# Kernel optimization log

Hardware: AMD Instinct MI355X
Metric: run time of the kernel (lower is better)

The kernel has to match this reference:

```python
import jax, jax.numpy as jnp
import numpy as np

N_NODES = 50000
N_RELS = 20          # raw relations; enriched total = 2*N_RELS + 1
N_EDGES = 500000
EMB = 16
N_CLASSES = 16
N_BASES = 40


def setup_inputs() -> dict:
    key = jax.random.key(0)
    ks = jax.random.split(key, 8)
    R_tot = 2 * N_RELS + 1
    src = jax.random.randint(ks[0], (N_EDGES,), 0, N_NODES)
    dst = jax.random.randint(ks[1], (N_EDGES,), 0, N_NODES)
    rel = jax.random.randint(ks[2], (N_EDGES,), 0, N_RELS)
    scale = 0.05
    comps1 = jax.random.normal(ks[3], (R_tot, N_BASES), jnp.float32) * scale
    bases1 = jax.random.normal(ks[4], (N_BASES, N_NODES, EMB), jnp.float32) * scale
    comps2 = jax.random.normal(ks[5], (R_tot, N_BASES), jnp.float32) * scale
    bases2 = jax.random.normal(ks[6], (N_BASES, EMB, N_CLASSES), jnp.float32) * scale
    bias1 = jnp.zeros((EMB,), jnp.float32)
    bias2 = jnp.zeros((N_CLASSES,), jnp.float32)
    return {"src": src, "dst": dst, "rel": rel,
            "comps1": comps1, "bases1": bases1,
            "comps2": comps2, "bases2": bases2,
            "bias1": bias1, "bias2": bias2}


def reference(src, dst, rel, comps1, bases1, comps2, bases2, bias1, bias2):
    N = bases1.shape[1]
    emb = bases1.shape[2]
    R_tot = comps1.shape[0]
    R = (R_tot - 1) // 2

    # enrich: originals + inverses + self-loops (relation 2R)
    loop = jnp.arange(N)
    s = jnp.concatenate([src, dst, loop])           # [E_tot]
    o = jnp.concatenate([dst, src, loop])
    r = jnp.concatenate([rel, rel + R, jnp.full((N,), 2 * R, rel.dtype)])

    # row-normalization of the vertical graph: value = 1 / count(row = r*N + s)
    seg = r * N + s
    cnt = jax.ops.segment_sum(jnp.ones_like(s, jnp.float32), seg,
                              num_segments=R_tot * N)
    v = 1.0 / cnt[seg]                               # [E_tot]

    # layer 1: basis-decomposed weights [R_tot, N, emb]
    w1 = jnp.einsum('rb,bne->rne', comps1, bases1)
    # hor_graph @ w1.view(R*N, emb): h[s] += v * w1[r, o]
    h = jnp.zeros((N, emb), w1.dtype).at[s].add(v[:, None] * w1[r, o])
    h = jax.nn.relu(h + bias1)

    # ver_graph @ h: hv[r, s] += v * h[o]  -> [R_tot, N, emb]
    hv = jnp.zeros((R_tot, N, emb), h.dtype).at[r, s].add(v[:, None] * h[o])

    # layer 2: basis-decomposed weights [R_tot, emb, C]; bmm + sum over relations
    w2 = jnp.einsum('rb,bec->rec', comps2, bases2)
    out = jnp.einsum('rne,rec->nc', hv, w2) + bias2  # [N, C]
    return out
```

## Files before the change

kernel.cpp:

```cpp
#include <hip/hip_runtime.h>

#define N_NODES 50000
#define N_RELSR 20
#define R_TOT   41
#define N_EDGES 500000
#define EMB     16
#define NCLS    16
#define NB      40
#define E_TOT   (2 * N_EDGES + N_NODES)
#define NE_COL  (N_NODES * EMB)
#define NBLK_N  ((N_NODES + 255) / 256)

__device__ __forceinline__ void edge_decode(int i, const int* __restrict__ src,
                                            const int* __restrict__ dst,
                                            const int* __restrict__ rel,
                                            int& s, int& o, int& r) {
    if (i < N_EDGES) {
        s = src[i]; o = dst[i]; r = rel[i];
    } else if (i < 2 * N_EDGES) {
        int j = i - N_EDGES;
        s = dst[j]; o = src[j]; r = rel[j] + N_RELSR;
    } else {
        int n = i - 2 * N_EDGES;
        s = n; o = n; r = 2 * N_RELSR;
    }
}


__global__ void k_count(const int* __restrict__ src, const int* __restrict__ dst,
                        const int* __restrict__ rel, int2* __restrict__ cnt2,
                        int* __restrict__ rank) {
    int i = blockIdx.x * blockDim.x + threadIdx.x;
    if (i >= E_TOT) return;
    int s, o, r;
    edge_decode(i, src, dst, rel, s, o, r);
    rank[i] = atomicAdd(&cnt2[r * N_NODES + s].x, 1);
}

__global__ void k_degA(int2* __restrict__ cnt2, int* __restrict__ deg,
                       int* __restrict__ bsum) {
    __shared__ int red[256];
    int t = threadIdx.x;
    int s = blockIdx.x * 256 + t;
    int run = 0;
    if (s < N_NODES) {
        for (int r = 0; r < R_TOT; r++) {
            int idx = r * N_NODES + s;
            int2 val = cnt2[idx];
            val.y = run;
            cnt2[idx] = val;
            run += val.x;
        }
        deg[s] = run;
    }
    red[t] = run;
    __syncthreads();
    for (int st = 128; st > 0; st >>= 1) {
        if (t < st) red[t] += red[t + st];
        __syncthreads();
    }
    if (t == 0) bsum[blockIdx.x] = red[0];
}

__global__ void k_degB(int* __restrict__ bsum) {
    __shared__ int sh[256];
    int t = threadIdx.x;
    int v = (t < NBLK_N) ? bsum[t] : 0;
    sh[t] = v;
    __syncthreads();
    for (int d = 1; d < 256; d <<= 1) {
        int x = (t >= d) ? sh[t - d] : 0;
        __syncthreads();
        sh[t] += x;
        __syncthreads();
    }
    if (t < NBLK_N) bsum[t] = sh[t] - v;
}

__global__ void k_degC(const int* __restrict__ deg, const int* __restrict__ bsum,
                       int* __restrict__ off, int2* __restrict__ cnt2) {
    __shared__ int sh[256];
    int t = threadIdx.x;
    int s = blockIdx.x * 256 + t;
    int d = (s < N_NODES) ? deg[s] : 0;
    sh[t] = d;
    __syncthreads();
    for (int dd = 1; dd < 256; dd <<= 1) {
        int x = (t >= dd) ? sh[t - dd] : 0;
        __syncthreads();
        sh[t] += x;
        __syncthreads();
    }
    int excl = sh[t] - d + bsum[blockIdx.x];
    if (s < N_NODES) {
        off[s] = excl;
        int* base = (int*)cnt2;
        for (int r = 0; r < R_TOT; r++) {
            base[2 * (r * N_NODES + s) + 1] += excl;
        }
    }
    if (s == 0) off[N_NODES] = E_TOT;
}

__global__ void k_fill(const int* __restrict__ src, const int* __restrict__ dst,
                       const int* __restrict__ rel, const int2* __restrict__ cnt2,
                       const int* __restrict__ rank, int2* __restrict__ recs) {
    int i = blockIdx.x * blockDim.x + threadIdx.x;
    if (i >= E_TOT) return;
    int s, o, r;
    edge_decode(i, src, dst, rel, s, o, r);
    int2 cr = cnt2[r * N_NODES + s];
    float v = 1.0f / (float)cr.x;
    recs[cr.y + rank[i]] = make_int2((r << 16) | o, __float_as_int(v));
}

__global__ void __launch_bounds__(256, 2)
k_w1(const float* __restrict__ comps1, const float* __restrict__ bases1,
     float* __restrict__ w1) {
    int j = blockIdx.x * blockDim.x + threadIdx.x;
    if (j >= NE_COL / 2) return;
    const float2* b2 = (const float2*)bases1;
    float2 acc[R_TOT];
#pragma unroll
    for (int r = 0; r < R_TOT; r++) { acc[r].x = 0.f; acc[r].y = 0.f; }
    for (int b = 0; b < NB; b++) {
        float2 bb = b2[(size_t)b * (NE_COL / 2) + j];
#pragma unroll
        for (int r = 0; r < R_TOT; r++) {
            float cc = comps1[r * NB + b];
            acc[r].x += cc * bb.x;
            acc[r].y += cc * bb.y;
        }
    }
    float2* w1p = (float2*)w1;
#pragma unroll
    for (int r = 0; r < R_TOT; r++) w1p[(size_t)r * (NE_COL / 2) + j] = acc[r];
}

__global__ void k_w2(const float* __restrict__ comps2, const float* __restrict__ bases2,
                     float* __restrict__ w2t) {
    int r = blockIdx.x;
    int t = threadIdx.x;
    int c = t >> 4, e = t & 15;
    float acc = 0.f;
#pragma unroll 8
    for (int b = 0; b < NB; b++) acc += comps2[r * NB + b] * bases2[b * (EMB * NCLS) + e * NCLS + c];
    w2t[r * (EMB * NCLS) + t] = acc;
}

__global__ void k_l1_gather(const int* __restrict__ off, const int2* __restrict__ recs,
                            const float* __restrict__ w1, const float* __restrict__ bias1,
                            float* __restrict__ h) {
    int t = blockIdx.x * blockDim.x + threadIdx.x;
    int s = t >> 4, e = t & 15;
    int beg = off[s], end = off[s + 1];
    float acc = 0.f;
    int j = beg;
    for (; j + 3 < end; j += 4) {
        int2 r0 = recs[j], r1 = recs[j + 1], r2 = recs[j + 2], r3 = recs[j + 3];
        float f0 = w1[(size_t)(r0.x >> 16) * NE_COL + (r0.x & 0xFFFF) * EMB + e];
        float f1 = w1[(size_t)(r1.x >> 16) * NE_COL + (r1.x & 0xFFFF) * EMB + e];
        float f2 = w1[(size_t)(r2.x >> 16) * NE_COL + (r2.x & 0xFFFF) * EMB + e];
        float f3 = w1[(size_t)(r3.x >> 16) * NE_COL + (r3.x & 0xFFFF) * EMB + e];
        acc += __int_as_float(r0.y) * f0 + __int_as_float(r1.y) * f1 +
               __int_as_float(r2.y) * f2 + __int_as_float(r3.y) * f3;
    }
    for (; j < end; j++) {
        int2 rc = recs[j];
        acc += __int_as_float(rc.y) *
               w1[(size_t)(rc.x >> 16) * NE_COL + (rc.x & 0xFFFF) * EMB + e];
    }
    h[t] = fmaxf(acc + bias1[e], 0.f);
}

__global__ void k_l1_gather_fly(const int* __restrict__ off, const int2* __restrict__ recs,
                                const float* __restrict__ comps1,
                                const float* __restrict__ bases1,
                                const float* __restrict__ bias1, float* __restrict__ h) {
    __shared__ float c1[R_TOT * NB];
    for (int q = threadIdx.x; q < R_TOT * NB; q += blockDim.x) c1[q] = comps1[q];
    __syncthreads();
    int t = blockIdx.x * blockDim.x + threadIdx.x;
    int s = t >> 4, e = t & 15;
    int beg = off[s], end = off[s + 1];
    float acc = 0.f;
    for (int j = beg; j < end; j++) {
        int2 rec = recs[j];
        int o = rec.x & 0xFFFF, r = rec.x >> 16;
        float v = __int_as_float(rec.y);
        const float* cr = &c1[r * NB];
        float w = 0.f;
#pragma unroll 8
        for (int b = 0; b < NB; b++) w += cr[b] * bases1[(size_t)b * NE_COL + o * EMB + e];
        acc += v * w;
    }
    h[t] = fmaxf(acc + bias1[e], 0.f);
}

#define W2C 20
#define W2R (16 * W2C + 4)
__global__ void k_l2_gather(const int* __restrict__ off, const int2* __restrict__ recs,
                            const float* __restrict__ h, const float* __restrict__ w2t,
                            const float* __restrict__ bias2, float* __restrict__ out) {
    __shared__ __align__(16) float w2s[R_TOT * W2R];
    for (int q = threadIdx.x; q < R_TOT * (EMB * NCLS); q += blockDim.x) {
        int r = q >> 8;
        int x = q & 255;
        int c = x >> 4, e = x & 15;
        w2s[r * W2R + c * W2C + e] = w2t[q];
    }
    __syncthreads();
    int t = blockIdx.x * blockDim.x + threadIdx.x;
    if (t >= NE_COL) return;
    int s = t >> 4, c = t & 15;
    int beg = off[s], end = off[s + 1];
    int cbase = c * W2C;
    float acc = 0.f;
    int j = beg;
    for (; j + 1 < end; j += 2) {
        int2 ra = recs[j], rb = recs[j + 1];
        const float4* ha = (const float4*)(h + (size_t)(ra.x & 0xFFFF) * EMB);
        const float4* hb = (const float4*)(h + (size_t)(rb.x & 0xFFFF) * EMB);
        float4 h0 = ha[0], h1 = ha[1], h2 = ha[2], h3 = ha[3];
        float4 g0 = hb[0], g1 = hb[1], g2 = hb[2], g3 = hb[3];
        const float4* wa = (const float4*)&w2s[(ra.x >> 16) * W2R + cbase];
        const float4* wb = (const float4*)&w2s[(rb.x >> 16) * W2R + cbase];
        float4 a0 = wa[0], a1 = wa[1], a2 = wa[2], a3 = wa[3];
        float4 b0 = wb[0], b1 = wb[1], b2 = wb[2], b3 = wb[3];
        float da, db;
        da  = h0.x * a0.x; da = fmaf(h0.y, a0.y, da); da = fmaf(h0.z, a0.z, da); da = fmaf(h0.w, a0.w, da);
        da = fmaf(h1.x, a1.x, da); da = fmaf(h1.y, a1.y, da); da = fmaf(h1.z, a1.z, da); da = fmaf(h1.w, a1.w, da);
        da = fmaf(h2.x, a2.x, da); da = fmaf(h2.y, a2.y, da); da = fmaf(h2.z, a2.z, da); da = fmaf(h2.w, a2.w, da);
        da = fmaf(h3.x, a3.x, da); da = fmaf(h3.y, a3.y, da); da = fmaf(h3.z, a3.z, da); da = fmaf(h3.w, a3.w, da);
        db  = g0.x * b0.x; db = fmaf(g0.y, b0.y, db); db = fmaf(g0.z, b0.z, db); db = fmaf(g0.w, b0.w, db);
        db = fmaf(g1.x, b1.x, db); db = fmaf(g1.y, b1.y, db); db = fmaf(g1.z, b1.z, db); db = fmaf(g1.w, b1.w, db);
        db = fmaf(g2.x, b2.x, db); db = fmaf(g2.y, b2.y, db); db = fmaf(g2.z, b2.z, db); db = fmaf(g2.w, b2.w, db);
        db = fmaf(g3.x, b3.x, db); db = fmaf(g3.y, b3.y, db); db = fmaf(g3.z, b3.z, db); db = fmaf(g3.w, b3.w, db);
        acc = fmaf(__int_as_float(ra.y), da, acc);
        acc = fmaf(__int_as_float(rb.y), db, acc);
    }
    for (; j < end; j++) {
        int2 ra = recs[j];
        const float4* ha = (const float4*)(h + (size_t)(ra.x & 0xFFFF) * EMB);
        float4 h0 = ha[0], h1 = ha[1], h2 = ha[2], h3 = ha[3];
        const float4* wa = (const float4*)&w2s[(ra.x >> 16) * W2R + cbase];
        float4 a0 = wa[0], a1 = wa[1], a2 = wa[2], a3 = wa[3];
        float da;
        da  = h0.x * a0.x; da = fmaf(h0.y, a0.y, da); da = fmaf(h0.z, a0.z, da); da = fmaf(h0.w, a0.w, da);
        da = fmaf(h1.x, a1.x, da); da = fmaf(h1.y, a1.y, da); da = fmaf(h1.z, a1.z, da); da = fmaf(h1.w, a1.w, da);
        da = fmaf(h2.x, a2.x, da); da = fmaf(h2.y, a2.y, da); da = fmaf(h2.z, a2.z, da); da = fmaf(h2.w, a2.w, da);
        da = fmaf(h3.x, a3.x, da); da = fmaf(h3.y, a3.y, da); da = fmaf(h3.z, a3.z, da); da = fmaf(h3.w, a3.w, da);
        acc = fmaf(__int_as_float(ra.y), da, acc);
    }
    out[s * NCLS + c] = acc + bias2[c];
}

static inline size_t align64(size_t x) { return (x + 63) & ~(size_t)63; }

extern "C" void kernel_launch(void* const* d_in, const int* in_sizes, int n_in,
                              void* d_out, int out_size, void* d_ws, size_t ws_size,
                              hipStream_t stream) {
    const int*   src    = (const int*)d_in[0];
    const int*   dst    = (const int*)d_in[1];
    const int*   rel    = (const int*)d_in[2];
    const float* comps1 = (const float*)d_in[3];
    const float* bases1 = (const float*)d_in[4];
    const float* comps2 = (const float*)d_in[5];
    const float* bases2 = (const float*)d_in[6];
    const float* bias1  = (const float*)d_in[7];
    const float* bias2  = (const float*)d_in[8];
    float* out = (float*)d_out;
    (void)in_sizes; (void)n_in; (void)out_size;

    char* ws = (char*)d_ws;
    size_t off_b = 0;
    float* w1   = (float*)ws;
    int2*  cnt2 = (int2*)ws;
    int*   rank = (int*)(ws + align64((size_t)R_TOT * N_NODES * 8));
    off_b = align64((size_t)R_TOT * NE_COL * 4);
    int*   deg  = (int*)(ws + off_b);  off_b = align64(off_b + (size_t)N_NODES * 4);
    int*   off  = (int*)(ws + off_b);  off_b = align64(off_b + (size_t)(N_NODES + 1) * 4);
    int*   bsum = (int*)(ws + off_b);  off_b = align64(off_b + (size_t)256 * 4);
    int2*  recs = (int2*)(ws + off_b); off_b = align64(off_b + (size_t)E_TOT * 8);
    float* h    = (float*)(ws + off_b); off_b = align64(off_b + (size_t)NE_COL * 4);
    float* w2t  = (float*)(ws + off_b); off_b = align64(off_b + (size_t)R_TOT * EMB * NCLS * 4);
    const bool materialize_w1 = (ws_size >= off_b);
    if (!materialize_w1) {
        off_b = 0;
        cnt2 = (int2*)(ws + off_b);  off_b = align64(off_b + (size_t)R_TOT * N_NODES * 8);
        rank = (int*)(ws + off_b);   off_b = align64(off_b + (size_t)E_TOT * 4);
        deg  = (int*)(ws + off_b);   off_b = align64(off_b + (size_t)N_NODES * 4);
        off  = (int*)(ws + off_b);   off_b = align64(off_b + (size_t)(N_NODES + 1) * 4);
        bsum = (int*)(ws + off_b);   off_b = align64(off_b + (size_t)256 * 4);
        recs = (int2*)(ws + off_b);  off_b = align64(off_b + (size_t)E_TOT * 8);
        h    = (float*)(ws + off_b); off_b = align64(off_b + (size_t)NE_COL * 4);
        w2t  = (float*)(ws + off_b); off_b = align64(off_b + (size_t)R_TOT * EMB * NCLS * 4);
    }

    hipMemsetAsync(cnt2, 0, (size_t)R_TOT * N_NODES * 8, stream);

    const int BLK = 256;
    const int g_edge = (E_TOT + BLK - 1) / BLK;
    const int g_w1   = (NE_COL / 2 + BLK - 1) / BLK;
    const int g_l1   = (N_NODES * 16) / BLK;
    const int g_l2   = (NE_COL + 511) / 512;

    k_count<<<g_edge, BLK, 0, stream>>>(src, dst, rel, cnt2, rank);
    k_degA<<<NBLK_N, 256, 0, stream>>>(cnt2, deg, bsum);
    k_degB<<<1, 256, 0, stream>>>(bsum);
    k_degC<<<NBLK_N, 256, 0, stream>>>(deg, bsum, off, cnt2);
    k_fill<<<g_edge, BLK, 0, stream>>>(src, dst, rel, cnt2, rank, recs);
    k_w2<<<R_TOT, EMB * NCLS, 0, stream>>>(comps2, bases2, w2t);

    if (materialize_w1) {
        k_w1<<<g_w1, BLK, 0, stream>>>(comps1, bases1, w1);
        k_l1_gather<<<g_l1, BLK, 0, stream>>>(off, recs, w1, bias1, h);
    } else {
        k_l1_gather_fly<<<g_l1, BLK, 0, stream>>>(off, recs, comps1, bases1, bias1, h);
    }

    k_l2_gather<<<g_l2, 512, 0, stream>>>(off, recs, h, w2t, bias2, out);
}
```

Measured before the change: 433.8 us.

## Store materialized layer-1 weights as bf16 and drop per-relation offset fixup

The materialized w1 table (41×50000×16) is now written as packed bf16 instead of fp32, halving its write traffic in k_w1 and the gather traffic in k_l1_gather. The per-row offset is also no longer added into cnt2 for every relation in k_degC; k_fill reads off[s] directly instead. This cuts a strided read-modify-write pass over cnt2 at the cost of one extra load per edge. Casting the weights to bf16 reduces accuracy of the layer-1 results, and the smaller workspace footprint may let materialization be chosen more often.

```diff
diff --git a/kernel.cpp b/kernel.cpp
--- a/kernel.cpp
+++ b/kernel.cpp
@@ -10,6 +10,15 @@
 #define E_TOT   (2 * N_EDGES + N_NODES)
 #define NE_COL  (N_NODES * EMB)
 #define NBLK_N  ((N_NODES + 255) / 256)
+
+__device__ __forceinline__ unsigned short f2bf(float f) {
+    unsigned u = __float_as_uint(f);
+    u += 0x7FFFu + ((u >> 16) & 1u);
+    return (unsigned short)(u >> 16);
+}
+__device__ __forceinline__ float bf2f(unsigned short b) {
+    return __uint_as_float((unsigned)b << 16);
+}
 
 __device__ __forceinline__ void edge_decode(int i, const int* __restrict__ src,
                                             const int* __restrict__ dst,
@@ -78,7 +87,7 @@
 }
 
 __global__ void k_degC(const int* __restrict__ deg, const int* __restrict__ bsum,
-                       int* __restrict__ off, int2* __restrict__ cnt2) {
+                       int* __restrict__ off) {
     __shared__ int sh[256];
     int t = threadIdx.x;
     int s = blockIdx.x * 256 + t;
@@ -92,31 +101,26 @@
         __syncthreads();
     }
     int excl = sh[t] - d + bsum[blockIdx.x];
-    if (s < N_NODES) {
-        off[s] = excl;
-        int* base = (int*)cnt2;
-        for (int r = 0; r < R_TOT; r++) {
-            base[2 * (r * N_NODES + s) + 1] += excl;
-        }
-    }
+    if (s < N_NODES) off[s] = excl;
     if (s == 0) off[N_NODES] = E_TOT;
 }
 
 __global__ void k_fill(const int* __restrict__ src, const int* __restrict__ dst,
                        const int* __restrict__ rel, const int2* __restrict__ cnt2,
-                       const int* __restrict__ rank, int2* __restrict__ recs) {
+                       const int* __restrict__ rank, const int* __restrict__ off,
+                       int2* __restrict__ recs) {
     int i = blockIdx.x * blockDim.x + threadIdx.x;
     if (i >= E_TOT) return;
     int s, o, r;
     edge_decode(i, src, dst, rel, s, o, r);
     int2 cr = cnt2[r * N_NODES + s];
     float v = 1.0f / (float)cr.x;
-    recs[cr.y + rank[i]] = make_int2((r << 16) | o, __float_as_int(v));
+    recs[off[s] + cr.y + rank[i]] = make_int2((r << 16) | o, __float_as_int(v));
 }
 
 __global__ void __launch_bounds__(256, 2)
 k_w1(const float* __restrict__ comps1, const float* __restrict__ bases1,
-     float* __restrict__ w1) {
+     unsigned* __restrict__ w1p) {
     int j = blockIdx.x * blockDim.x + threadIdx.x;
     if (j >= NE_COL / 2) return;
     const float2* b2 = (const float2*)bases1;
@@ -132,9 +136,11 @@
             acc[r].y += cc * bb.y;
         }
     }
-    float2* w1p = (float2*)w1;
 #pragma unroll
-    for (int r = 0; r < R_TOT; r++) w1p[(size_t)r * (NE_COL / 2) + j] = acc[r];
+    for (int r = 0; r < R_TOT; r++) {
+        unsigned pk = ((unsigned)f2bf(acc[r].y) << 16) | (unsigned)f2bf(acc[r].x);
+        w1p[(size_t)r * (NE_COL / 2) + j] = pk;
+    }
 }
 
 __global__ void k_w2(const float* __restrict__ comps2, const float* __restrict__ bases2,
@@ -149,8 +155,8 @@
 }
 
 __global__ void k_l1_gather(const int* __restrict__ off, const int2* __restrict__ recs,
-                            const float* __restrict__ w1, const float* __restrict__ bias1,
-                            float* __restrict__ h) {
+                            const unsigned short* __restrict__ w1,
+                            const float* __restrict__ bias1, float* __restrict__ h) {
     int t = blockIdx.x * blockDim.x + threadIdx.x;
     int s = t >> 4, e = t & 15;
     int beg = off[s], end = off[s + 1];
@@ -158,17 +164,17 @@
     int j = beg;
     for (; j + 3 < end; j += 4) {
         int2 r0 = recs[j], r1 = recs[j + 1], r2 = recs[j + 2], r3 = recs[j + 3];
-        float f0 = w1[(size_t)(r0.x >> 16) * NE_COL + (r0.x & 0xFFFF) * EMB + e];
-        float f1 = w1[(size_t)(r1.x >> 16) * NE_COL + (r1.x & 0xFFFF) * EMB + e];
-        float f2 = w1[(size_t)(r2.x >> 16) * NE_COL + (r2.x & 0xFFFF) * EMB + e];
-        float f3 = w1[(size_t)(r3.x >> 16) * NE_COL + (r3.x & 0xFFFF) * EMB + e];
+        float f0 = bf2f(w1[(size_t)(r0.x >> 16) * NE_COL + (r0.x & 0xFFFF) * EMB + e]);
+        float f1 = bf2f(w1[(size_t)(r1.x >> 16) * NE_COL + (r1.x & 0xFFFF) * EMB + e]);
+        float f2 = bf2f(w1[(size_t)(r2.x >> 16) * NE_COL + (r2.x & 0xFFFF) * EMB + e]);
+        float f3 = bf2f(w1[(size_t)(r3.x >> 16) * NE_COL + (r3.x & 0xFFFF) * EMB + e]);
         acc += __int_as_float(r0.y) * f0 + __int_as_float(r1.y) * f1 +
                __int_as_float(r2.y) * f2 + __int_as_float(r3.y) * f3;
     }
     for (; j < end; j++) {
         int2 rc = recs[j];
         acc += __int_as_float(rc.y) *
-               w1[(size_t)(rc.x >> 16) * NE_COL + (rc.x & 0xFFFF) * EMB + e];
+               bf2f(w1[(size_t)(rc.x >> 16) * NE_COL + (rc.x & 0xFFFF) * EMB + e]);
     }
     h[t] = fmaxf(acc + bias1[e], 0.f);
 }
@@ -274,10 +280,10 @@
 
     char* ws = (char*)d_ws;
     size_t off_b = 0;
-    float* w1   = (float*)ws;
+    unsigned short* w1 = (unsigned short*)ws;
     int2*  cnt2 = (int2*)ws;
     int*   rank = (int*)(ws + align64((size_t)R_TOT * N_NODES * 8));
-    off_b = align64((size_t)R_TOT * NE_COL * 4);
+    off_b = align64((size_t)R_TOT * NE_COL * 2);
     int*   deg  = (int*)(ws + off_b);  off_b = align64(off_b + (size_t)N_NODES * 4);
     int*   off  = (int*)(ws + off_b);  off_b = align64(off_b + (size_t)(N_NODES + 1) * 4);
     int*   bsum = (int*)(ws + off_b);  off_b = align64(off_b + (size_t)256 * 4);
@@ -308,12 +314,12 @@
     k_count<<<g_edge, BLK, 0, stream>>>(src, dst, rel, cnt2, rank);
     k_degA<<<NBLK_N, 256, 0, stream>>>(cnt2, deg, bsum);
     k_degB<<<1, 256, 0, stream>>>(bsum);
-    k_degC<<<NBLK_N, 256, 0, stream>>>(deg, bsum, off, cnt2);
-    k_fill<<<g_edge, BLK, 0, stream>>>(src, dst, rel, cnt2, rank, recs);
+    k_degC<<<NBLK_N, 256, 0, stream>>>(deg, bsum, off);
+    k_fill<<<g_edge, BLK, 0, stream>>>(src, dst, rel, cnt2, rank, off, recs);
     k_w2<<<R_TOT, EMB * NCLS, 0, stream>>>(comps2, bases2, w2t);
 
     if (materialize_w1) {
-        k_w1<<<g_w1, BLK, 0, stream>>>(comps1, bases1, w1);
+        k_w1<<<g_w1, BLK, 0, stream>>>(comps1, bases1, (unsigned*)w1);
         k_l1_gather<<<g_l1, BLK, 0, stream>>>(off, recs, w1, bias1, h);
     } else {
         k_l1_gather_fly<<<g_l1, BLK, 0, stream>>>(off, recs, comps1, bases1, bias1, h);
```

After: 412.4 us. -4.9%, faster.
